# Kernel optimization log

Measured on AMD Instinct MI355X. Metric: run time of the kernel, lower is better.

Reference implementation:

```python
import jax, jax.numpy as jnp
import numpy as np

TOP_K = 8
N_EXPERTS = 64
EPS = 1e-6

def setup_inputs() -> dict:
    key = jax.random.key(0)
    k1, k2 = jax.random.split(key)
    tokens, dim = 16384, 4096
    x = jax.random.normal(k1, (tokens, dim), dtype=jnp.float32)
    gate_w = jax.random.normal(k2, (N_EXPERTS, dim), dtype=jnp.float32) * (1.0 / np.sqrt(dim))
    expert_bias = jnp.zeros((N_EXPERTS,), dtype=jnp.float32)
    return {"x": x, "gate_w": gate_w, "expert_bias": expert_bias}

def reference(x, gate_w, expert_bias):
    # logits: (tokens, n_experts)
    logits = jnp.einsum('td,ed->te', x, gate_w) + expert_bias
    scores = jax.nn.sigmoid(logits)
    scores = scores / (jnp.sum(scores, axis=-1, keepdims=True) + EPS)
    weights, indices = jax.lax.top_k(scores, TOP_K)  # (tokens, top_k)
    weights = weights / (jnp.sum(weights, axis=-1, keepdims=True) + EPS)
    # load balance loss
    n_tokens = scores.shape[0]
    one_hot = jax.nn.one_hot(indices, N_EXPERTS, dtype=jnp.float32)  # (tokens, top_k, E)
    tokens_per_expert = jnp.sum(one_hot, axis=(0, 1)) / n_tokens  # (E,)
    avg_prob = jnp.mean(scores, axis=0)  # (E,)
    loss = N_EXPERTS * jnp.sum(tokens_per_expert * avg_prob)
    return (weights, indices, loss)
```

## Files before the change

kernel.cpp:

```cpp
#include <hip/hip_runtime.h>
#include <math.h>


constexpr int DIM     = 4096;
constexpr int NE      = 64;
constexpr int TOPK    = 8;
constexpr float EPS   = 1e-6f;
constexpr int TPB_TOK = 16;
constexpr int KC      = 256;

__device__ inline double shfl_xor_d(double v, int off) {
    long long x = __double_as_longlong(v);
    int lo = (int)(unsigned int)(x & 0xffffffffLL);
    int hi = (int)(x >> 32);
    lo = __shfl_xor(lo, off);
    hi = __shfl_xor(hi, off);
    long long y = ((long long)hi << 32) | (unsigned int)lo;
    return __longlong_as_double(y);
}

__global__ __launch_bounds__(256)
void transpose_gw(const float* __restrict__ gw, double2* __restrict__ gwd2)
{
    int idx = blockIdx.x * 256 + threadIdx.x;
    int e  = idx & 63;
    int k2 = idx >> 6;
    float g0 = gw[(size_t)e * DIM + 2 * k2];
    float g1 = gw[(size_t)e * DIM + 2 * k2 + 1];
    double2 d; d.x = (double)g0; d.y = (double)g1;
    gwd2[idx] = d;
}

__global__ __launch_bounds__(256, 4)
void router_main(const float* __restrict__ x, const double2* __restrict__ gwd2,
                 const float* __restrict__ bias, float* __restrict__ out,
                 float* __restrict__ ws_ssum, float* __restrict__ ws_cnt,
                 int tokens)
{
    __shared__ double xt[TPB_TOK][KC];
    __shared__ float red_s[4][NE];
    __shared__ float red_c[4][NE];

    const int tid  = threadIdx.x;
    const int wave = tid >> 6;
    const int lane = tid & 63;
    const int tok0 = blockIdx.x * TPB_TOK;
    const int wtok = tok0 + wave * 4;
    const int w4   = wave * 4;

    double accA0 = 0, accA1 = 0, accA2 = 0, accA3 = 0;
    double accB0 = 0, accB1 = 0, accB2 = 0, accB3 = 0;

    const double2* gbase = gwd2 + lane;

    for (int kc = 0; kc < DIM; kc += KC) {
        __syncthreads();
        #pragma unroll
        for (int i = 0; i < 4; ++i) {
            int r  = i * 4 + wave;
            int c4 = lane;
            float4 v = *reinterpret_cast<const float4*>(
                &x[(size_t)(tok0 + r) * DIM + kc + c4 * 4]);
            double2 d0; d0.x = (double)v.x; d0.y = (double)v.y;
            double2 d1; d1.x = (double)v.z; d1.y = (double)v.w;
            *reinterpret_cast<double2*>(&xt[r][c4 * 4 + 0]) = d0;
            *reinterpret_cast<double2*>(&xt[r][c4 * 4 + 2]) = d1;
        }
        __syncthreads();

        const int k2base = kc >> 1;
        #pragma unroll 4
        for (int k2 = 0; k2 < KC / 2; k2 += 2) {
            double2 g0 = gbase[(size_t)(k2base + k2) * 64];
            double2 g1 = gbase[(size_t)(k2base + k2 + 1) * 64];
            double2 a0 = *reinterpret_cast<const double2*>(&xt[w4 + 0][2 * k2]);
            double2 b0 = *reinterpret_cast<const double2*>(&xt[w4 + 0][2 * k2 + 2]);
            accA0 = fma(g0.x, a0.x, accA0); accA0 = fma(g0.y, a0.y, accA0);
            accB0 = fma(g1.x, b0.x, accB0); accB0 = fma(g1.y, b0.y, accB0);
            double2 a1 = *reinterpret_cast<const double2*>(&xt[w4 + 1][2 * k2]);
            double2 b1 = *reinterpret_cast<const double2*>(&xt[w4 + 1][2 * k2 + 2]);
            accA1 = fma(g0.x, a1.x, accA1); accA1 = fma(g0.y, a1.y, accA1);
            accB1 = fma(g1.x, b1.x, accB1); accB1 = fma(g1.y, b1.y, accB1);
            double2 a2 = *reinterpret_cast<const double2*>(&xt[w4 + 2][2 * k2]);
            double2 b2 = *reinterpret_cast<const double2*>(&xt[w4 + 2][2 * k2 + 2]);
            accA2 = fma(g0.x, a2.x, accA2); accA2 = fma(g0.y, a2.y, accA2);
            accB2 = fma(g1.x, b2.x, accB2); accB2 = fma(g1.y, b2.y, accB2);
            double2 a3 = *reinterpret_cast<const double2*>(&xt[w4 + 3][2 * k2]);
            double2 b3 = *reinterpret_cast<const double2*>(&xt[w4 + 3][2 * k2 + 2]);
            accA3 = fma(g0.x, a3.x, accA3); accA3 = fma(g0.y, a3.y, accA3);
            accB3 = fma(g1.x, b3.x, accB3); accB3 = fma(g1.y, b3.y, accB3);
        }
    }

    const double b = (double)bias[lane];
    double dl[4] = {accA0 + accB0 + b, accA1 + accB1 + b,
                    accA2 + accB2 + b, accA3 + accB3 + b};

    float my_ssum = 0.f;
    float my_cnt  = 0.f;

    #pragma unroll
    for (int j = 0; j < 4; ++j) {
        float sig = 1.f / (1.f + expf(-(float)dl[j]));
        float S = sig;
        #pragma unroll
        for (int off = 32; off; off >>= 1) S += __shfl_xor(S, off);
        float ns = sig / (S + EPS);
        my_ssum += ns;

        double key = dl[j];
        float topsum = 0.f;
        float myval  = 0.f;
        int   myidx  = 0;
        #pragma unroll
        for (int k = 0; k < TOPK; ++k) {
            double kv = key; int id = lane;
            #pragma unroll
            for (int off = 32; off; off >>= 1) {
                double okv = shfl_xor_d(kv, off);
                int    oi  = __shfl_xor(id, off);
                if (okv > kv || (okv == kv && oi < id)) { kv = okv; id = oi; }
            }
            float nsw = __shfl(ns, id);
            topsum += nsw;
            if (lane == k)  { myval = nsw; myidx = id; }
            if (lane == id) { key = -1.0e300; my_cnt += 1.f; }
        }
        float wnorm = myval / (topsum + EPS);
        int tok = wtok + j;
        if (lane < TOPK) {
            out[(size_t)tok * TOPK + lane] = wnorm;
            out[(size_t)tokens * TOPK + (size_t)tok * TOPK + lane] = (float)myidx;
        }
    }

    red_s[wave][lane] = my_ssum;
    red_c[wave][lane] = my_cnt;
    __syncthreads();
    if (tid < NE) {
        float s = red_s[0][tid] + red_s[1][tid] + red_s[2][tid] + red_s[3][tid];
        float c = red_c[0][tid] + red_c[1][tid] + red_c[2][tid] + red_c[3][tid];
        ws_ssum[(size_t)blockIdx.x * NE + tid] = s;
        ws_cnt [(size_t)blockIdx.x * NE + tid] = c;
    }
}

__global__ __launch_bounds__(256)
void router_loss(const float* __restrict__ ws_ssum, const float* __restrict__ ws_cnt,
                 float* __restrict__ out, int nblocks, int tokens)
{
    __shared__ float ps[4][NE];
    __shared__ float pc[4][NE];
    const int e  = threadIdx.x & 63;
    const int sl = threadIdx.x >> 6;
    float s = 0.f, c = 0.f;
    for (int bb = sl; bb < nblocks; bb += 4) {
        s += ws_ssum[(size_t)bb * NE + e];
        c += ws_cnt [(size_t)bb * NE + e];
    }
    ps[sl][e] = s; pc[sl][e] = c;
    __syncthreads();
    if (threadIdx.x < NE) {
        float st = ps[0][e] + ps[1][e] + ps[2][e] + ps[3][e];
        float ct = pc[0][e] + pc[1][e] + pc[2][e] + pc[3][e];
        float prod = st * ct;
        #pragma unroll
        for (int off = 32; off; off >>= 1) prod += __shfl_xor(prod, off);
        if (threadIdx.x == 0) {
            float T = (float)tokens;
            out[(size_t)tokens * TOPK * 2] = (float)NE * prod / (T * T);
        }
    }
}

extern "C" void kernel_launch(void* const* d_in, const int* in_sizes, int n_in,
                              void* d_out, int out_size, void* d_ws, size_t ws_size,
                              hipStream_t stream)
{
    const float* x    = (const float*)d_in[0];
    const float* gw   = (const float*)d_in[1];
    const float* bias = (const float*)d_in[2];
    float* out = (float*)d_out;

    const int tokens  = in_sizes[0] / DIM;
    const int nblocks = tokens / TPB_TOK;

    double2* gwd2  = (double2*)d_ws;
    float* ws_ssum = (float*)((char*)d_ws + (size_t)(DIM / 2) * NE * sizeof(double2));
    float* ws_cnt  = ws_ssum + (size_t)nblocks * NE;

    transpose_gw<<<(DIM / 2) * NE / 256, 256, 0, stream>>>(gw, gwd2);
    router_main<<<nblocks, 256, 0, stream>>>(x, gwd2, bias, out, ws_ssum, ws_cnt, tokens);
    router_loss<<<1, 256, 0, stream>>>(ws_ssum, ws_cnt, out, nblocks, tokens);
}
```

Before: 790.2 us.

## Compute router logits in fp32 and recompute near-tie tokens in fp64

The main GEMV now runs in fp32 with the x tile read directly from global memory, with no LDS staging. Each wave handles 8 tokens, and a per-lane transposed float4 copy of gate_w serves as the weight input. Tokens whose top-9 logit gaps fall below a tolerance are added to a flag list through an atomic, and a new repair kernel recomputes their logits and top-k in fp64. This avoids the slow fp64 FMA throughput for most tokens, at the cost of an extra kernel and reliance on the tolerance catching every ordering flip. The load-balance loss is still built from the fp32 scores and counts, and the repair pass does not correct them.

```diff
diff --git a/kernel.cpp b/kernel.cpp
--- a/kernel.cpp
+++ b/kernel.cpp
@@ -6,13 +6,17 @@
 constexpr int NE      = 64;
 constexpr int TOPK    = 8;
 constexpr float EPS   = 1e-6f;
-constexpr int TPB_TOK = 16;
-constexpr int KC      = 256;
+constexpr float TAU   = 1e-4f;
+constexpr int T       = 8;
+constexpr int WPB     = 4;
+constexpr int TPB_TOK = T * WPB;
+constexpr int MAXFLAG = 16384;
+constexpr int REPAIR_WAVES = 2048;
 
 __device__ inline double shfl_xor_d(double v, int off) {
-    long long x = __double_as_longlong(v);
-    int lo = (int)(unsigned int)(x & 0xffffffffLL);
-    int hi = (int)(x >> 32);
+    long long xx = __double_as_longlong(v);
+    int lo = (int)(unsigned int)(xx & 0xffffffffLL);
+    int hi = (int)(xx >> 32);
     lo = __shfl_xor(lo, off);
     hi = __shfl_xor(hi, off);
     long long y = ((long long)hi << 32) | (unsigned int)lo;
@@ -20,98 +24,148 @@
 }
 
 __global__ __launch_bounds__(256)
-void transpose_gw(const float* __restrict__ gw, double2* __restrict__ gwd2)
-{
-    int idx = blockIdx.x * 256 + threadIdx.x;
-    int e  = idx & 63;
-    int k2 = idx >> 6;
-    float g0 = gw[(size_t)e * DIM + 2 * k2];
-    float g1 = gw[(size_t)e * DIM + 2 * k2 + 1];
-    double2 d; d.x = (double)g0; d.y = (double)g1;
-    gwd2[idx] = d;
-}
-
-__global__ __launch_bounds__(256, 4)
-void router_main(const float* __restrict__ x, const double2* __restrict__ gwd2,
+void prep(const float* __restrict__ gw, float4* __restrict__ gwT4,
+          double2* __restrict__ gwd2, int* __restrict__ flag_cnt)
+{
+    int g  = blockIdx.x * 256 + threadIdx.x;
+    int e  = g >> 10;
+    int k4 = g & 1023;
+    float4 v = *reinterpret_cast<const float4*>(&gw[(size_t)e * DIM + 4 * k4]);
+    gwT4[(size_t)k4 * NE + e] = v;
+    double2 d0; d0.x = (double)v.x; d0.y = (double)v.y;
+    double2 d1; d1.x = (double)v.z; d1.y = (double)v.w;
+    gwd2[(size_t)(2 * k4)     * NE + e] = d0;
+    gwd2[(size_t)(2 * k4 + 1) * NE + e] = d1;
+    if (g == 0) *flag_cnt = 0;
+}
+
+__global__ __launch_bounds__(256)
+void router_main(const float* __restrict__ x, const float4* __restrict__ gwT4,
                  const float* __restrict__ bias, float* __restrict__ out,
                  float* __restrict__ ws_ssum, float* __restrict__ ws_cnt,
+                 int* __restrict__ flag_cnt, int* __restrict__ flag_list,
                  int tokens)
 {
-    __shared__ double xt[TPB_TOK][KC];
-    __shared__ float red_s[4][NE];
-    __shared__ float red_c[4][NE];
+    __shared__ float red_s[WPB][NE];
+    __shared__ float red_c[WPB][NE];
 
     const int tid  = threadIdx.x;
     const int wave = tid >> 6;
     const int lane = tid & 63;
-    const int tok0 = blockIdx.x * TPB_TOK;
-    const int wtok = tok0 + wave * 4;
-    const int w4   = wave * 4;
-
-    double accA0 = 0, accA1 = 0, accA2 = 0, accA3 = 0;
-    double accB0 = 0, accB1 = 0, accB2 = 0, accB3 = 0;
-
-    const double2* gbase = gwd2 + lane;
-
-    for (int kc = 0; kc < DIM; kc += KC) {
-        __syncthreads();
-        #pragma unroll
-        for (int i = 0; i < 4; ++i) {
-            int r  = i * 4 + wave;
-            int c4 = lane;
-            float4 v = *reinterpret_cast<const float4*>(
-                &x[(size_t)(tok0 + r) * DIM + kc + c4 * 4]);
-            double2 d0; d0.x = (double)v.x; d0.y = (double)v.y;
-            double2 d1; d1.x = (double)v.z; d1.y = (double)v.w;
-            *reinterpret_cast<double2*>(&xt[r][c4 * 4 + 0]) = d0;
-            *reinterpret_cast<double2*>(&xt[r][c4 * 4 + 2]) = d1;
-        }
-        __syncthreads();
-
-        const int k2base = kc >> 1;
-        #pragma unroll 4
-        for (int k2 = 0; k2 < KC / 2; k2 += 2) {
-            double2 g0 = gbase[(size_t)(k2base + k2) * 64];
-            double2 g1 = gbase[(size_t)(k2base + k2 + 1) * 64];
-            double2 a0 = *reinterpret_cast<const double2*>(&xt[w4 + 0][2 * k2]);
-            double2 b0 = *reinterpret_cast<const double2*>(&xt[w4 + 0][2 * k2 + 2]);
-            accA0 = fma(g0.x, a0.x, accA0); accA0 = fma(g0.y, a0.y, accA0);
-            accB0 = fma(g1.x, b0.x, accB0); accB0 = fma(g1.y, b0.y, accB0);
-            double2 a1 = *reinterpret_cast<const double2*>(&xt[w4 + 1][2 * k2]);
-            double2 b1 = *reinterpret_cast<const double2*>(&xt[w4 + 1][2 * k2 + 2]);
-            accA1 = fma(g0.x, a1.x, accA1); accA1 = fma(g0.y, a1.y, accA1);
-            accB1 = fma(g1.x, b1.x, accB1); accB1 = fma(g1.y, b1.y, accB1);
-            double2 a2 = *reinterpret_cast<const double2*>(&xt[w4 + 2][2 * k2]);
-            double2 b2 = *reinterpret_cast<const double2*>(&xt[w4 + 2][2 * k2 + 2]);
-            accA2 = fma(g0.x, a2.x, accA2); accA2 = fma(g0.y, a2.y, accA2);
-            accB2 = fma(g1.x, b2.x, accB2); accB2 = fma(g1.y, b2.y, accB2);
-            double2 a3 = *reinterpret_cast<const double2*>(&xt[w4 + 3][2 * k2]);
-            double2 b3 = *reinterpret_cast<const double2*>(&xt[w4 + 3][2 * k2 + 2]);
-            accA3 = fma(g0.x, a3.x, accA3); accA3 = fma(g0.y, a3.y, accA3);
-            accB3 = fma(g1.x, b3.x, accB3); accB3 = fma(g1.y, b3.y, accB3);
-        }
-    }
-
-    const double b = (double)bias[lane];
-    double dl[4] = {accA0 + accB0 + b, accA1 + accB1 + b,
-                    accA2 + accB2 + b, accA3 + accB3 + b};
-
-    float my_ssum = 0.f;
-    float my_cnt  = 0.f;
-
+    const int wtok = __builtin_amdgcn_readfirstlane(blockIdx.x * TPB_TOK + wave * T);
+    const float* xb = x + (size_t)wtok * DIM;
+    const float4* gp = gwT4 + lane;
+
+    float acc[T];
     #pragma unroll
-    for (int j = 0; j < 4; ++j) {
-        float sig = 1.f / (1.f + expf(-(float)dl[j]));
+    for (int t = 0; t < T; ++t) acc[t] = 0.f;
+
+    #pragma unroll 2
+    for (int k4 = 0; k4 < DIM / 4; ++k4) {
+        float4 gv = gp[(size_t)k4 * NE];
+        #pragma unroll
+        for (int t = 0; t < T; ++t) {
+            float4 xv = *reinterpret_cast<const float4*>(xb + (size_t)t * DIM + 4 * k4);
+            acc[t] = fmaf(gv.x, xv.x, acc[t]);
+            acc[t] = fmaf(gv.y, xv.y, acc[t]);
+            acc[t] = fmaf(gv.z, xv.z, acc[t]);
+            acc[t] = fmaf(gv.w, xv.w, acc[t]);
+        }
+    }
+
+    const float b = bias[lane];
+    float my_ssum = 0.f, my_cnt = 0.f;
+
+    #pragma unroll 1
+    for (int t = 0; t < T; ++t) {
+        float logit = acc[t] + b;
+        float sig = 1.f / (1.f + expf(-logit));
         float S = sig;
         #pragma unroll
         for (int off = 32; off; off >>= 1) S += __shfl_xor(S, off);
         float ns = sig / (S + EPS);
         my_ssum += ns;
 
-        double key = dl[j];
-        float topsum = 0.f;
-        float myval  = 0.f;
-        int   myidx  = 0;
+        float key = logit;
+        float topsum = 0.f, myval = 0.f;
+        int   myidx = 0;
+        float prevv = 0.f, mingap = 1e30f;
+        #pragma unroll
+        for (int k = 0; k < TOPK + 1; ++k) {
+            float v = key; int id = lane;
+            #pragma unroll
+            for (int off = 32; off; off >>= 1) {
+                float ov = __shfl_xor(v, off);
+                int   oi = __shfl_xor(id, off);
+                if (ov > v || (ov == v && oi < id)) { v = ov; id = oi; }
+            }
+            if (k > 0) mingap = fminf(mingap, prevv - v);
+            prevv = v;
+            if (k < TOPK) {
+                float nsw = __shfl(ns, id);
+                topsum += nsw;
+                if (lane == k)  { myval = nsw; myidx = id; }
+                if (lane == id) { key = -1e30f; my_cnt += 1.f; }
+            }
+        }
+        int tok = wtok + t;
+        float wnorm = myval / (topsum + EPS);
+        if (lane < TOPK) {
+            out[(size_t)tok * TOPK + lane] = wnorm;
+            out[(size_t)tokens * TOPK + (size_t)tok * TOPK + lane] = (float)myidx;
+        }
+        if (lane == 0 && mingap < TAU) {
+            int p = atomicAdd(flag_cnt, 1);
+            if (p < MAXFLAG) flag_list[p] = tok;
+        }
+    }
+
+    red_s[wave][lane] = my_ssum;
+    red_c[wave][lane] = my_cnt;
+    __syncthreads();
+    if (tid < NE) {
+        float s = red_s[0][tid] + red_s[1][tid] + red_s[2][tid] + red_s[3][tid];
+        float c = red_c[0][tid] + red_c[1][tid] + red_c[2][tid] + red_c[3][tid];
+        ws_ssum[(size_t)blockIdx.x * NE + tid] = s;
+        ws_cnt [(size_t)blockIdx.x * NE + tid] = c;
+    }
+}
+
+__global__ __launch_bounds__(256)
+void router_repair(const float* __restrict__ x, const double2* __restrict__ gwd2,
+                   const float* __restrict__ bias, float* __restrict__ out,
+                   const int* __restrict__ flag_cnt, const int* __restrict__ flag_list,
+                   int tokens)
+{
+    const int lane = threadIdx.x & 63;
+    const int wid  = __builtin_amdgcn_readfirstlane(
+                        (int)((blockIdx.x * 256 + threadIdx.x) >> 6));
+    int n = *flag_cnt;
+    if (n > MAXFLAG) n = MAXFLAG;
+
+    for (int i = wid; i < n; i += REPAIR_WAVES) {
+        const int tok = __builtin_amdgcn_readfirstlane(flag_list[i]);
+        const float* xr = x + (size_t)tok * DIM;
+        const double2* gb = gwd2 + lane;
+        double acc = 0.0;
+        for (int k2 = 0; k2 < DIM / 2; ++k2) {
+            double2 g = gb[(size_t)k2 * NE];
+            float x0 = xr[2 * k2];
+            float x1 = xr[2 * k2 + 1];
+            acc = fma((double)x0, g.x, acc);
+            acc = fma((double)x1, g.y, acc);
+        }
+        double dl = acc + (double)bias[lane];
+
+        float sig = 1.f / (1.f + expf(-(float)dl));
+        float S = sig;
+        #pragma unroll
+        for (int off = 32; off; off >>= 1) S += __shfl_xor(S, off);
+        float ns = sig / (S + EPS);
+
+        double key = dl;
+        float topsum = 0.f, myval = 0.f;
+        int   myidx = 0;
         #pragma unroll
         for (int k = 0; k < TOPK; ++k) {
             double kv = key; int id = lane;
@@ -124,24 +178,12 @@
             float nsw = __shfl(ns, id);
             topsum += nsw;
             if (lane == k)  { myval = nsw; myidx = id; }
-            if (lane == id) { key = -1.0e300; my_cnt += 1.f; }
-        }
-        float wnorm = myval / (topsum + EPS);
-        int tok = wtok + j;
+            if (lane == id) key = -1.0e300;
+        }
         if (lane < TOPK) {
-            out[(size_t)tok * TOPK + lane] = wnorm;
+            out[(size_t)tok * TOPK + lane] = myval / (topsum + EPS);
             out[(size_t)tokens * TOPK + (size_t)tok * TOPK + lane] = (float)myidx;
         }
-    }
-
-    red_s[wave][lane] = my_ssum;
-    red_c[wave][lane] = my_cnt;
-    __syncthreads();
-    if (tid < NE) {
-        float s = red_s[0][tid] + red_s[1][tid] + red_s[2][tid] + red_s[3][tid];
-        float c = red_c[0][tid] + red_c[1][tid] + red_c[2][tid] + red_c[3][tid];
-        ws_ssum[(size_t)blockIdx.x * NE + tid] = s;
-        ws_cnt [(size_t)blockIdx.x * NE + tid] = c;
     }
 }
 
@@ -167,8 +209,8 @@
         #pragma unroll
         for (int off = 32; off; off >>= 1) prod += __shfl_xor(prod, off);
         if (threadIdx.x == 0) {
-            float T = (float)tokens;
-            out[(size_t)tokens * TOPK * 2] = (float)NE * prod / (T * T);
+            float Tn = (float)tokens;
+            out[(size_t)tokens * TOPK * 2] = (float)NE * prod / (Tn * Tn);
         }
     }
 }
@@ -185,11 +227,18 @@
     const int tokens  = in_sizes[0] / DIM;
     const int nblocks = tokens / TPB_TOK;
 
-    double2* gwd2  = (double2*)d_ws;
-    float* ws_ssum = (float*)((char*)d_ws + (size_t)(DIM / 2) * NE * sizeof(double2));
-    float* ws_cnt  = ws_ssum + (size_t)nblocks * NE;
-
-    transpose_gw<<<(DIM / 2) * NE / 256, 256, 0, stream>>>(gw, gwd2);
-    router_main<<<nblocks, 256, 0, stream>>>(x, gwd2, bias, out, ws_ssum, ws_cnt, tokens);
+    char* wsb = (char*)d_ws;
+    float4*  gwT4     = (float4*) (wsb);
+    double2* gwd2     = (double2*)(wsb + (1u << 20));
+    int*     flag_cnt = (int*)    (wsb + (3u << 20));
+    int*     flag_list= (int*)    (wsb + (3u << 20) + 64);
+    float*   ws_ssum  = (float*)  (wsb + (3u << 20) + 64 + MAXFLAG * sizeof(int));
+    float*   ws_cnt   = ws_ssum + (size_t)nblocks * NE;
+
+    prep<<<NE * (DIM / 4) / 256, 256, 0, stream>>>(gw, gwT4, gwd2, flag_cnt);
+    router_main<<<nblocks, 256, 0, stream>>>(x, gwT4, bias, out, ws_ssum, ws_cnt,
+                                             flag_cnt, flag_list, tokens);
+    router_repair<<<REPAIR_WAVES / 4, 256, 0, stream>>>(x, gwd2, bias, out,
+                                                        flag_cnt, flag_list, tokens);
     router_loss<<<1, 256, 0, stream>>>(ws_ssum, ws_cnt, out, nblocks, tokens);
 }
```

Measured after the change: 1.065 ms. 34.8% more time.
